# Performance work log

Measured on AMD Instinct MI355X. Metric: run time of the kernel, lower is better.

## Reference

```python
import jax, jax.numpy as jnp
import numpy as np

IN_CAPS = 128      # number of memory capsules (rows of m)
NUM_CAPS = 5       # n_class
DIM_CAPS = 153     # comp_dim // n_class = 768 // 5
IN_DIM = 768       # comp_dim
NQ = 256           # number of query samples
NUM_ROUTING = 3
BETA = 1.0         # config['Model']['temperature']
EPS = 1e-8


def _pearsonr(x, y):
    # Pearson correlation along last dim (broadcasts over leading dims).
    xm = x - x.mean(axis=-1, keepdims=True)
    ym = y - y.mean(axis=-1, keepdims=True)
    num = (xm * ym).sum(axis=-1)
    den = jnp.sqrt((xm * xm).sum(axis=-1)) * jnp.sqrt((ym * ym).sum(axis=-1))
    return num / (den + EPS)


def _squash(s):
    # capsule squash along last dim
    n2 = (s * s).sum(axis=-1, keepdims=True)
    return (n2 / (1.0 + n2)) * s / jnp.sqrt(n2 + EPS)


def setup_inputs() -> dict:
    key = jax.random.key(0)
    k1, k2, k3 = jax.random.split(key, 3)
    m = jax.random.normal(k1, (IN_CAPS, IN_DIM), dtype=jnp.float32)
    q = jax.random.normal(k2, (NQ, IN_DIM), dtype=jnp.float32)
    W = jax.random.normal(k3, (IN_DIM, NUM_CAPS * DIM_CAPS), dtype=jnp.float32) * 0.02
    b = jnp.zeros((NUM_CAPS * DIM_CAPS,), dtype=jnp.float32)
    return {"m": m, "q": q, "W": W, "b": b}


def reference(m, q, W, b):
    sg = jax.lax.stop_gradient
    # projections -> capsule preactivations
    hat_m = (m @ W + b).reshape(IN_CAPS, NUM_CAPS, DIM_CAPS)          # [I,C,D]
    hat_q = (q @ W + b).reshape(-1, NUM_CAPS, DIM_CAPS)               # [Q,C,D]
    Qn = hat_q.shape[0]
    tmp_m = sg(hat_m)[None, :, :, :]                                   # [1,I,C,D] (broadcast over Q)
    tmp_q = sg(hat_q)[:, None, :, :]                                   # [Q,1,C,D]

    a = jnp.zeros((Qn, IN_CAPS, NUM_CAPS), dtype=hat_q.dtype)          # routing logits
    p = jnp.tanh(_pearsonr(tmp_m, tmp_q))                              # [Q,I,C]

    for _ in range(NUM_ROUTING - 1):
        d = jax.nn.softmax(a / BETA, axis=2)                           # [Q,I,C]
        dsp = d + p
        hat_v = (tmp_m * dsp[..., None]).sum(axis=1)                   # [Q,C,D]
        v = _squash(hat_v)
        m_dot_v = (tmp_m * v[:, None, :, :]).sum(axis=-1)              # [Q,I,C]
        a = a + p * m_dot_v
        tmp_q = (tmp_q + v[:, None, :, :]) * 0.5                       # [Q,I,C,D]
        p = jnp.tanh(_pearsonr(tmp_m, tmp_q))

    d = jax.nn.softmax(a / BETA, axis=2)
    dsp = sg(d + p)                                                    # routing coeffs detached
    hat_v = (hat_m[None, :, :, :] * dsp[..., None]).sum(axis=1)        # grad flows via hat_m only
    q_prime = _squash(hat_v).reshape(Qn, -1)                           # [Q, C*D]
    return q_prime
```

## Files before the change

kernel.cpp:

```cpp
#include <hip/hip_runtime.h>
#include <hip/hip_bf16.h>

#define I_CAPS 128
#define N_CAPS 5
#define D_CAPS 153
#define D_PAD  160
#define MLD    800
#define IN_DIM 768
#define NQ     256
#define CD     765
#define NPAIR  640
#define EPSF   1e-8f
#define KHALF  384

typedef __hip_bfloat16 bf16;

__device__ __forceinline__ float wred(float x) {
#pragma unroll
  for (int off = 32; off; off >>= 1) x += __shfl_down(x, off, 64);
  return x;
}

__device__ __forceinline__ float tanh_fast(float x) {
  float t = __expf(-2.f * fabsf(x));
  float r = (1.f - t) / (1.f + t);
  return copysignf(r, x);
}

__device__ __forceinline__ int is_bf16(const unsigned* __restrict__ m_u32) {
  int lane = threadIdx.x & 63;
  unsigned u = m_u32[lane];
  int e = (u >> 7) & 0xFF;
  unsigned long long mask = __ballot(e >= 118 && e <= 134);
  return __popcll(mask) >= 48;
}

template <bool ISB>
__device__ __forceinline__ float ld_in(const void* p, long idx) {
  if (ISB) return __bfloat162float(((const bf16*)p)[idx]);
  return ((const float*)p)[idx];
}

template <bool ISB>
__device__ void gemm_body(const void* m, const void* q, const void* W,
                          const void* b, float* hat_m, float* hat_q) {
  __shared__ float As[8][KHALF];
  const int tx = threadIdx.x, ty = threadIdx.y;
  const int t = ty * 64 + tx;
  const int row0 = blockIdx.y * 8;
  const int k0 = blockIdx.z * KHALF;

  if (ISB) {
    for (int e = t; e < 8 * KHALF; e += 256) {
      int rr = e / KHALF, kk = e - rr * KHALF;
      int row = row0 + rr;
      As[rr][kk] = (row < I_CAPS)
                       ? ld_in<true>(m, (long)row * IN_DIM + k0 + kk)
                       : ld_in<true>(q, (long)(row - I_CAPS) * IN_DIM + k0 + kk);
    }
  } else {
    for (int e = t; e < 8 * (KHALF / 4); e += 256) {
      int rr = e / (KHALF / 4), k4 = e - rr * (KHALF / 4);
      int row = row0 + rr;
      const float* src = (row < I_CAPS)
                             ? (const float*)m + (long)row * IN_DIM
                             : (const float*)q + (long)(row - I_CAPS) * IN_DIM;
      *(float4*)&As[rr][k4 * 4] = *(const float4*)(src + k0 + k4 * 4);
    }
  }
  __syncthreads();

  const int col = blockIdx.x * 64 + tx;
  const int colc = (col < CD) ? col : (CD - 1);
  const int r0 = ty * 2, r1 = r0 + 1;

  float a0a = 0.f, a0b = 0.f, a1a = 0.f, a1b = 0.f;
#pragma unroll 2
  for (int k = 0; k < KHALF; k += 8) {
    const float4 A0a = *(const float4*)&As[r0][k];
    const float4 A0b = *(const float4*)&As[r0][k + 4];
    const float4 A1a = *(const float4*)&As[r1][k];
    const float4 A1b = *(const float4*)&As[r1][k + 4];
    float w0 = ld_in<ISB>(W, (long)(k0 + k + 0) * CD + colc);
    float w1 = ld_in<ISB>(W, (long)(k0 + k + 1) * CD + colc);
    float w2 = ld_in<ISB>(W, (long)(k0 + k + 2) * CD + colc);
    float w3 = ld_in<ISB>(W, (long)(k0 + k + 3) * CD + colc);
    float w4 = ld_in<ISB>(W, (long)(k0 + k + 4) * CD + colc);
    float w5 = ld_in<ISB>(W, (long)(k0 + k + 5) * CD + colc);
    float w6 = ld_in<ISB>(W, (long)(k0 + k + 6) * CD + colc);
    float w7 = ld_in<ISB>(W, (long)(k0 + k + 7) * CD + colc);
    a0a = fmaf(A0a.x, w0, a0a); a0b = fmaf(A0a.y, w1, a0b);
    a0a = fmaf(A0a.z, w2, a0a); a0b = fmaf(A0a.w, w3, a0b);
    a0a = fmaf(A0b.x, w4, a0a); a0b = fmaf(A0b.y, w5, a0b);
    a0a = fmaf(A0b.z, w6, a0a); a0b = fmaf(A0b.w, w7, a0b);
    a1a = fmaf(A1a.x, w0, a1a); a1b = fmaf(A1a.y, w1, a1b);
    a1a = fmaf(A1a.z, w2, a1a); a1b = fmaf(A1a.w, w3, a1b);
    a1a = fmaf(A1b.x, w4, a1a); a1b = fmaf(A1b.y, w5, a1b);
    a1a = fmaf(A1b.z, w6, a1a); a1b = fmaf(A1b.w, w7, a1b);
  }

  if (col < CD) {
    float p0 = a0a + a0b;
    float p1 = a1a + a1b;
    if (blockIdx.z == 0) {
      float bias = ld_in<ISB>(b, col);
      p0 += bias;
      p1 += bias;
    }
    int c = col / D_CAPS, d = col - c * D_CAPS;
    int ra = row0 + r0, rb = row0 + r1;
    float* d0 = (ra < I_CAPS) ? &hat_m[ra * MLD + c * D_PAD + d]
                              : &hat_q[(ra - I_CAPS) * CD + col];
    float* d1 = (rb < I_CAPS) ? &hat_m[rb * MLD + c * D_PAD + d]
                              : &hat_q[(rb - I_CAPS) * CD + col];
    atomicAdd(d0, p0);
    atomicAdd(d1, p1);
  }
}

__global__ __launch_bounds__(256, 4)
void gemm_kernel(const void* m, const void* q, const void* W, const void* b,
                 float* __restrict__ hat_m, float* __restrict__ hat_q) {
  if (is_bf16((const unsigned*)m))
    gemm_body<true>(m, q, W, b, hat_m, hat_q);
  else
    gemm_body<false>(m, q, W, b, hat_m, hat_q);
}

__global__ __launch_bounds__(128)
void gram_kernel(const float* __restrict__ hat_m, float* __restrict__ G,
                 float* __restrict__ mean_m, float* __restrict__ ssm) {
  const int c = blockIdx.x, j = blockIdx.y, i = threadIdx.x;
  const float4* hi = (const float4*)(hat_m + i * MLD + c * D_PAD);
  const float4* hj = (const float4*)(hat_m + j * MLD + c * D_PAD);
  float a0 = 0.f, a1 = 0.f, a2 = 0.f, a3 = 0.f;
  float s = 0.f;
#pragma unroll 8
  for (int k = 0; k < 40; ++k) {
    float4 x = hi[k];
    float4 y = hj[k];
    a0 = fmaf(x.x, y.x, a0);
    a1 = fmaf(x.y, y.y, a1);
    a2 = fmaf(x.z, y.z, a2);
    a3 = fmaf(x.w, y.w, a3);
    s += (x.x + x.y) + (x.z + x.w);
  }
  float dot = (a0 + a1) + (a2 + a3);
  G[c * 16384 + j * 128 + i] = dot;
  if (i == j) {
    float mu = s * (1.f / D_CAPS);
    mean_m[j * N_CAPS + c] = mu;
    ssm[j * N_CAPS + c] = fmaxf(dot - (float)D_CAPS * mu * mu, 0.f);
  }
}

__global__ __launch_bounds__(1024, 4)
void routing_kernel(const float* __restrict__ hat_m,
                    const float* __restrict__ hat_q,
                    const float* __restrict__ Gmat,
                    const float* __restrict__ mean_m,
                    const float* __restrict__ ssm,
                    const unsigned* __restrict__ m_u32,
                    void* __restrict__ out_v) {
  __shared__ float tq[N_CAPS * D_PAD], vv[N_CAPS * D_PAD];
  __shared__ float aa[NPAIR], pp[NPAIR], dsp[NPAIR], sdot[NPAIR];
  __shared__ float smm[NPAIR], sss[NPAIR];
  __shared__ float meanq[N_CAPS], ssq[N_CAPS], sc_s[N_CAPS];
  __shared__ float tsum_s[N_CAPS], t2_s[N_CAPS];
  __shared__ float red[10][4];

  const int tid = threadIdx.x;
  const int qi = blockIdx.x;
  const int w = tid >> 6, lane = tid & 63;
  const int g = tid >> 3, sub = tid & 7;
  const float* hq = hat_q + qi * CD;
  const float* hm = hat_m + g * MLD;

  for (int l = tid; l < N_CAPS * D_PAD; l += 1024) {
    int c = l / D_PAD, d = l - c * D_PAD;
    tq[l] = (d < D_CAPS) ? hq[c * D_CAPS + d] : 0.f;
  }
  if (tid < NPAIR) {
    aa[tid] = 0.f;
    smm[tid] = mean_m[tid];
    sss[tid] = ssm[tid];
  }
  __syncthreads();

  if (w < N_CAPS) {
    const int c = w;
    float s = 0.f, s2 = 0.f;
    for (int d = lane; d < D_CAPS; d += 64) {
      float x = tq[c * D_PAD + d];
      s += x;
      s2 = fmaf(x, x, s2);
    }
    s = wred(s);
    s2 = wred(s2);
    if (lane == 0) {
      float mu = s * (1.f / D_CAPS);
      tsum_s[c] = s;
      t2_s[c] = s2;
      meanq[c] = mu;
      ssq[c] = fmaxf(s2 - (float)D_CAPS * mu * mu, 0.f);
    }
  }
  __syncthreads();

  {
    float A0 = 0.f, A1 = 0.f, A2 = 0.f, A3 = 0.f, A4 = 0.f;
#pragma unroll 2
    for (int jj = 0; jj < 5; ++jj) {
      int d = jj * 32 + sub * 4;
      float4 h0 = *(const float4*)(hm + 0 * D_PAD + d);
      float4 h1 = *(const float4*)(hm + 1 * D_PAD + d);
      float4 h2 = *(const float4*)(hm + 2 * D_PAD + d);
      float4 h3 = *(const float4*)(hm + 3 * D_PAD + d);
      float4 h4 = *(const float4*)(hm + 4 * D_PAD + d);
      float4 t0 = *(const float4*)(tq + 0 * D_PAD + d);
      float4 t1 = *(const float4*)(tq + 1 * D_PAD + d);
      float4 t2 = *(const float4*)(tq + 2 * D_PAD + d);
      float4 t3 = *(const float4*)(tq + 3 * D_PAD + d);
      float4 t4 = *(const float4*)(tq + 4 * D_PAD + d);
      A0 = fmaf(h0.x, t0.x, A0); A0 = fmaf(h0.y, t0.y, A0);
      A0 = fmaf(h0.z, t0.z, A0); A0 = fmaf(h0.w, t0.w, A0);
      A1 = fmaf(h1.x, t1.x, A1); A1 = fmaf(h1.y, t1.y, A1);
      A1 = fmaf(h1.z, t1.z, A1); A1 = fmaf(h1.w, t1.w, A1);
      A2 = fmaf(h2.x, t2.x, A2); A2 = fmaf(h2.y, t2.y, A2);
      A2 = fmaf(h2.z, t2.z, A2); A2 = fmaf(h2.w, t2.w, A2);
      A3 = fmaf(h3.x, t3.x, A3); A3 = fmaf(h3.y, t3.y, A3);
      A3 = fmaf(h3.z, t3.z, A3); A3 = fmaf(h3.w, t3.w, A3);
      A4 = fmaf(h4.x, t4.x, A4); A4 = fmaf(h4.y, t4.y, A4);
      A4 = fmaf(h4.z, t4.z, A4); A4 = fmaf(h4.w, t4.w, A4);
    }
#pragma unroll
    for (int off = 1; off < 8; off <<= 1) {
      A0 += __shfl_xor(A0, off, 64);
      A1 += __shfl_xor(A1, off, 64);
      A2 += __shfl_xor(A2, off, 64);
      A3 += __shfl_xor(A3, off, 64);
      A4 += __shfl_xor(A4, off, 64);
    }
    if (sub < N_CAPS) {
      float acc = A0;
      acc = (sub == 1) ? A1 : acc;
      acc = (sub == 2) ? A2 : acc;
      acc = (sub == 3) ? A3 : acc;
      acc = (sub == 4) ? A4 : acc;
      int ic = g * N_CAPS + sub;
      sdot[ic] = acc;
      float num = acc - (float)D_CAPS * smm[ic] * meanq[sub];
      float den = sqrtf(sss[ic]) * sqrtf(ssq[sub]) + EPSF;
      pp[ic] = tanh_fast(num / den);
    }
  }
  __syncthreads();

  auto softmax_dsp = [&]() {
    if (tid < I_CAPS) {
      float av[N_CAPS], ev[N_CAPS];
      float mx = -1e30f;
#pragma unroll
      for (int c = 0; c < N_CAPS; ++c) {
        av[c] = aa[tid * N_CAPS + c];
        mx = fmaxf(mx, av[c]);
      }
      float s = 0.f;
#pragma unroll
      for (int c = 0; c < N_CAPS; ++c) {
        ev[c] = __expf(av[c] - mx);
        s += ev[c];
      }
      float inv = 1.f / s;
#pragma unroll
      for (int c = 0; c < N_CAPS; ++c)
        dsp[tid * N_CAPS + c] = ev[c] * inv + pp[tid * N_CAPS + c];
    }
  };

  for (int r = 0; r < 2; ++r) {
    softmax_dsp();
    __syncthreads();
    float y = 0.f, sold = 0.f;
    int cc = 0, ii = 0, ic = 0;
    if (tid < NPAIR) {
      cc = tid >> 7;
      ii = tid & 127;
      ic = ii * N_CAPS + cc;
      const float* Gp = Gmat + cc * 16384 + ii;
      float y0 = 0.f, y1 = 0.f;
#pragma unroll 4
      for (int j = 0; j < 128; j += 2) {
        y0 = fmaf(Gp[j * 128], dsp[j * N_CAPS + cc], y0);
        y1 = fmaf(Gp[(j + 1) * 128], dsp[(j + 1) * N_CAPS + cc], y1);
      }
      y = y0 + y1;
      sold = sdot[ic];
      float dmy = dsp[ic];
      float n2p = wred(dmy * y);
      float vsp = wred(dmy * ((float)D_CAPS * smm[ic]));
      float sdp = wred(dmy * sold);
      if (lane == 0) {
        red[w][0] = n2p;
        red[w][1] = vsp;
        red[w][2] = sdp;
      }
    }
    __syncthreads();
    if (tid < N_CAPS) {
      float n2 = red[2 * tid][0] + red[2 * tid + 1][0];
      float vs = red[2 * tid][1] + red[2 * tid + 1][1];
      float sd = red[2 * tid][2] + red[2 * tid + 1][2];
      float sc = (n2 / (1.f + n2)) * rsqrtf(n2 + EPSF);
      sc_s[tid] = sc;
      float ts = 0.5f * (tsum_s[tid] + sc * vs);
      float t2 = 0.25f * (t2_s[tid] + 2.f * sc * sd + sc * sc * n2);
      tsum_s[tid] = ts;
      t2_s[tid] = t2;
      float mu = ts * (1.f / D_CAPS);
      meanq[tid] = mu;
      ssq[tid] = fmaxf(t2 - (float)D_CAPS * mu * mu, 0.f);
    }
    __syncthreads();
    if (tid < NPAIR) {
      float mdv = sc_s[cc] * y;
      aa[ic] += pp[ic] * mdv;
      float snew = 0.5f * (sold + mdv);
      sdot[ic] = snew;
      float num = snew - (float)D_CAPS * smm[ic] * meanq[cc];
      float den = sqrtf(sss[ic]) * sqrtf(ssq[cc]) + EPSF;
      pp[ic] = tanh_fast(num / den);
    }
    __syncthreads();
  }

  softmax_dsp();
  __syncthreads();
  for (int cd = tid; cd < CD; cd += 1024) {
    int c = cd / D_CAPS, d = cd - c * D_CAPS;
    const float* col = hat_m + c * D_PAD + d;
    float b0 = 0.f, b1 = 0.f, b2 = 0.f, b3 = 0.f;
    float b4 = 0.f, b5 = 0.f, b6 = 0.f, b7 = 0.f;
#pragma unroll 4
    for (int i = 0; i < I_CAPS; i += 8) {
      b0 = fmaf(dsp[(i + 0) * N_CAPS + c], col[(i + 0) * MLD], b0);
      b1 = fmaf(dsp[(i + 1) * N_CAPS + c], col[(i + 1) * MLD], b1);
      b2 = fmaf(dsp[(i + 2) * N_CAPS + c], col[(i + 2) * MLD], b2);
      b3 = fmaf(dsp[(i + 3) * N_CAPS + c], col[(i + 3) * MLD], b3);
      b4 = fmaf(dsp[(i + 4) * N_CAPS + c], col[(i + 4) * MLD], b4);
      b5 = fmaf(dsp[(i + 5) * N_CAPS + c], col[(i + 5) * MLD], b5);
      b6 = fmaf(dsp[(i + 6) * N_CAPS + c], col[(i + 6) * MLD], b6);
      b7 = fmaf(dsp[(i + 7) * N_CAPS + c], col[(i + 7) * MLD], b7);
    }
    vv[c * D_PAD + d] = ((b0 + b1) + (b2 + b3)) + ((b4 + b5) + (b6 + b7));
  }
  __syncthreads();
  if (w < N_CAPS) {
    const int c = w;
    float s2 = 0.f;
    for (int d = lane; d < D_CAPS; d += 64) {
      float x = vv[c * D_PAD + d];
      s2 = fmaf(x, x, s2);
    }
    s2 = wred(s2);
    if (lane == 0) sc_s[c] = (s2 / (1.f + s2)) * rsqrtf(s2 + EPSF);
  }
  __syncthreads();

  int isb = is_bf16(m_u32);
  if (!isb) {
    float* out = (float*)out_v;
    for (int cd = tid; cd < CD; cd += 1024) {
      int c = cd / D_CAPS, d = cd - c * D_CAPS;
      out[qi * CD + cd] = vv[c * D_PAD + d] * sc_s[c];
    }
  } else {
    bf16* out = (bf16*)out_v;
    for (int cd = tid; cd < CD; cd += 1024) {
      int c = cd / D_CAPS, d = cd - c * D_CAPS;
      out[qi * CD + cd] = __float2bfloat16(vv[c * D_PAD + d] * sc_s[c]);
    }
  }
}

extern "C" void kernel_launch(void* const* d_in, const int* in_sizes, int n_in,
                              void* d_out, int out_size, void* d_ws, size_t ws_size,
                              hipStream_t stream) {
  const void *m = nullptr, *q = nullptr, *W = nullptr, *b = nullptr;
  for (int i = 0; i < n_in; ++i) {
    switch (in_sizes[i]) {
      case I_CAPS * IN_DIM: m = d_in[i]; break;
      case NQ * IN_DIM:     q = d_in[i]; break;
      case IN_DIM * CD:     W = d_in[i]; break;
      case CD:              b = d_in[i]; break;
      default: break;
    }
  }
  if (!m || !q || !W || !b) {
    m = d_in[0]; q = d_in[1]; W = d_in[2]; b = d_in[3];
  }

  float* mean_m = (float*)d_ws + 16;
  float* ssm    = mean_m + 640;
  float* hat_m  = ssm + 640;
  float* hat_q  = hat_m + I_CAPS * MLD;
  float* G      = hat_q + NQ * CD;

  hipMemsetAsync(hat_m, 0,
                 ((size_t)I_CAPS * MLD + (size_t)NQ * CD) * sizeof(float),
                 stream);
  gemm_kernel<<<dim3(12, 48, 2), dim3(64, 4), 0, stream>>>(m, q, W, b,
                                                           hat_m, hat_q);
  gram_kernel<<<dim3(N_CAPS, I_CAPS), 128, 0, stream>>>(hat_m, G,
                                                        mean_m, ssm);
  routing_kernel<<<NQ, 1024, 0, stream>>>(hat_m, hat_q, G, mean_m, ssm,
                                          (const unsigned*)m, d_out);
}
```

Measured before the change: 117.0 us.

## Drop split-K atomics and memset; read only valid capsule lanes in Gram

The projection GEMM no longer splits K across two blocks. Each block now covers the full 768-wide reduction and writes its outputs with plain stores, which removes the memset of the workspace and the float atomicAdds. Because the padding columns of hat_m are no longer zeroed, the Gram kernel now reads only the 153 valid elements (38 float4 loads plus one scalar tail) rather than 160. In exchange the GEMM launches half as many blocks and each runs a loop twice as long, with a larger shared-memory tile, which reduces parallelism and occupancy.

```diff
diff --git a/kernel.cpp b/kernel.cpp
--- a/kernel.cpp
+++ b/kernel.cpp
@@ -11,7 +11,6 @@
 #define CD     765
 #define NPAIR  640
 #define EPSF   1e-8f
-#define KHALF  384
 
 typedef __hip_bfloat16 bf16;
 
@@ -44,28 +43,27 @@
 template <bool ISB>
 __device__ void gemm_body(const void* m, const void* q, const void* W,
                           const void* b, float* hat_m, float* hat_q) {
-  __shared__ float As[8][KHALF];
+  __shared__ float As[8][IN_DIM];
   const int tx = threadIdx.x, ty = threadIdx.y;
   const int t = ty * 64 + tx;
   const int row0 = blockIdx.y * 8;
-  const int k0 = blockIdx.z * KHALF;
 
   if (ISB) {
-    for (int e = t; e < 8 * KHALF; e += 256) {
-      int rr = e / KHALF, kk = e - rr * KHALF;
+    for (int e = t; e < 8 * IN_DIM; e += 256) {
+      int rr = e / IN_DIM, kk = e - rr * IN_DIM;
       int row = row0 + rr;
       As[rr][kk] = (row < I_CAPS)
-                       ? ld_in<true>(m, (long)row * IN_DIM + k0 + kk)
-                       : ld_in<true>(q, (long)(row - I_CAPS) * IN_DIM + k0 + kk);
+                       ? ld_in<true>(m, (long)row * IN_DIM + kk)
+                       : ld_in<true>(q, (long)(row - I_CAPS) * IN_DIM + kk);
     }
   } else {
-    for (int e = t; e < 8 * (KHALF / 4); e += 256) {
-      int rr = e / (KHALF / 4), k4 = e - rr * (KHALF / 4);
+    for (int e = t; e < 8 * (IN_DIM / 4); e += 256) {
+      int rr = e / (IN_DIM / 4), k4 = e - rr * (IN_DIM / 4);
       int row = row0 + rr;
       const float* src = (row < I_CAPS)
                              ? (const float*)m + (long)row * IN_DIM
                              : (const float*)q + (long)(row - I_CAPS) * IN_DIM;
-      *(float4*)&As[rr][k4 * 4] = *(const float4*)(src + k0 + k4 * 4);
+      *(float4*)&As[rr][k4 * 4] = *(const float4*)(src + k4 * 4);
     }
   }
   __syncthreads();
@@ -76,19 +74,19 @@
 
   float a0a = 0.f, a0b = 0.f, a1a = 0.f, a1b = 0.f;
 #pragma unroll 2
-  for (int k = 0; k < KHALF; k += 8) {
+  for (int k = 0; k < IN_DIM; k += 8) {
     const float4 A0a = *(const float4*)&As[r0][k];
     const float4 A0b = *(const float4*)&As[r0][k + 4];
     const float4 A1a = *(const float4*)&As[r1][k];
     const float4 A1b = *(const float4*)&As[r1][k + 4];
-    float w0 = ld_in<ISB>(W, (long)(k0 + k + 0) * CD + colc);
-    float w1 = ld_in<ISB>(W, (long)(k0 + k + 1) * CD + colc);
-    float w2 = ld_in<ISB>(W, (long)(k0 + k + 2) * CD + colc);
-    float w3 = ld_in<ISB>(W, (long)(k0 + k + 3) * CD + colc);
-    float w4 = ld_in<ISB>(W, (long)(k0 + k + 4) * CD + colc);
-    float w5 = ld_in<ISB>(W, (long)(k0 + k + 5) * CD + colc);
-    float w6 = ld_in<ISB>(W, (long)(k0 + k + 6) * CD + colc);
-    float w7 = ld_in<ISB>(W, (long)(k0 + k + 7) * CD + colc);
+    float w0 = ld_in<ISB>(W, (long)(k + 0) * CD + colc);
+    float w1 = ld_in<ISB>(W, (long)(k + 1) * CD + colc);
+    float w2 = ld_in<ISB>(W, (long)(k + 2) * CD + colc);
+    float w3 = ld_in<ISB>(W, (long)(k + 3) * CD + colc);
+    float w4 = ld_in<ISB>(W, (long)(k + 4) * CD + colc);
+    float w5 = ld_in<ISB>(W, (long)(k + 5) * CD + colc);
+    float w6 = ld_in<ISB>(W, (long)(k + 6) * CD + colc);
+    float w7 = ld_in<ISB>(W, (long)(k + 7) * CD + colc);
     a0a = fmaf(A0a.x, w0, a0a); a0b = fmaf(A0a.y, w1, a0b);
     a0a = fmaf(A0a.z, w2, a0a); a0b = fmaf(A0a.w, w3, a0b);
     a0a = fmaf(A0b.x, w4, a0a); a0b = fmaf(A0b.y, w5, a0b);
@@ -100,21 +98,15 @@
   }
 
   if (col < CD) {
-    float p0 = a0a + a0b;
-    float p1 = a1a + a1b;
-    if (blockIdx.z == 0) {
-      float bias = ld_in<ISB>(b, col);
-      p0 += bias;
-      p1 += bias;
-    }
+    float bias = ld_in<ISB>(b, col);
+    float p0 = a0a + a0b + bias;
+    float p1 = a1a + a1b + bias;
     int c = col / D_CAPS, d = col - c * D_CAPS;
     int ra = row0 + r0, rb = row0 + r1;
-    float* d0 = (ra < I_CAPS) ? &hat_m[ra * MLD + c * D_PAD + d]
-                              : &hat_q[(ra - I_CAPS) * CD + col];
-    float* d1 = (rb < I_CAPS) ? &hat_m[rb * MLD + c * D_PAD + d]
-                              : &hat_q[(rb - I_CAPS) * CD + col];
-    atomicAdd(d0, p0);
-    atomicAdd(d1, p1);
+    if (ra < I_CAPS) hat_m[ra * MLD + c * D_PAD + d] = p0;
+    else             hat_q[(ra - I_CAPS) * CD + col] = p0;
+    if (rb < I_CAPS) hat_m[rb * MLD + c * D_PAD + d] = p1;
+    else             hat_q[(rb - I_CAPS) * CD + col] = p1;
   }
 }
 
@@ -131,12 +123,14 @@
 void gram_kernel(const float* __restrict__ hat_m, float* __restrict__ G,
                  float* __restrict__ mean_m, float* __restrict__ ssm) {
   const int c = blockIdx.x, j = blockIdx.y, i = threadIdx.x;
-  const float4* hi = (const float4*)(hat_m + i * MLD + c * D_PAD);
-  const float4* hj = (const float4*)(hat_m + j * MLD + c * D_PAD);
+  const float* hip_ = hat_m + i * MLD + c * D_PAD;
+  const float* hjp_ = hat_m + j * MLD + c * D_PAD;
+  const float4* hi = (const float4*)hip_;
+  const float4* hj = (const float4*)hjp_;
   float a0 = 0.f, a1 = 0.f, a2 = 0.f, a3 = 0.f;
   float s = 0.f;
 #pragma unroll 8
-  for (int k = 0; k < 40; ++k) {
+  for (int k = 0; k < 38; ++k) {
     float4 x = hi[k];
     float4 y = hj[k];
     a0 = fmaf(x.x, y.x, a0);
@@ -145,6 +139,9 @@
     a3 = fmaf(x.w, y.w, a3);
     s += (x.x + x.y) + (x.z + x.w);
   }
+  float xt = hip_[152], yt = hjp_[152];
+  a0 = fmaf(xt, yt, a0);
+  s += xt;
   float dot = (a0 + a1) + (a2 + a3);
   G[c * 16384 + j * 128 + i] = dot;
   if (i == j) {
@@ -406,11 +403,8 @@
   float* hat_q  = hat_m + I_CAPS * MLD;
   float* G      = hat_q + NQ * CD;
 
-  hipMemsetAsync(hat_m, 0,
-                 ((size_t)I_CAPS * MLD + (size_t)NQ * CD) * sizeof(float),
-                 stream);
-  gemm_kernel<<<dim3(12, 48, 2), dim3(64, 4), 0, stream>>>(m, q, W, b,
-                                                           hat_m, hat_q);
+  gemm_kernel<<<dim3(12, 48), dim3(64, 4), 0, stream>>>(m, q, W, b,
+                                                        hat_m, hat_q);
   gram_kernel<<<dim3(N_CAPS, I_CAPS), 128, 0, stream>>>(hat_m, G,
                                                         mean_m, ssm);
   routing_kernel<<<NQ, 1024, 0, stream>>>(hat_m, hat_q, G, mean_m, ssm,
```

Result: slower. 119.9 us (+2.5%).
